# Kernel optimization log

Measured on AMD Instinct MI355X. Metric: run time of the kernel, lower is better.

Reference implementation:

```python
import jax, jax.numpy as jnp
import numpy as np

EPS = 1e-15
LRELU_ALPHA = 0.2  # = init alpha


def setup_inputs() -> dict:
    key = jax.random.key(0)
    k1, k2, k3, k4 = jax.random.split(key, 4)
    N, E, F_in, F_out = 100000, 3200000, 256, 64
    inputs = jax.random.normal(k1, (N, F_in), dtype=jnp.float32)
    edge_index = jax.random.randint(k2, (2, E), 0, N, dtype=jnp.int64)
    # xavier_normal with gain 1.414
    W = jax.random.normal(k3, (F_in, F_out), dtype=jnp.float32) * (1.414 * np.sqrt(2.0 / (F_in + F_out)))
    a = jax.random.normal(k4, (1, 2 * F_out), dtype=jnp.float32) * (1.414 * np.sqrt(2.0 / (1 + 2 * F_out)))
    return {"inputs": inputs, "edge_index": edge_index, "W": W, "a": a}


def reference(inputs, edge_index, W, a):
    N = inputs.shape[0]
    F_out = W.shape[1]
    src = edge_index[0]  # row i (destination of aggregation)
    dst = edge_index[1]  # col j (neighbor being aggregated)

    h = inputs @ W  # [N, F_out]
    # values = a @ concat(h[src], h[dst]).T  ==  (h @ a1)[src] + (h @ a2)[dst]
    a1 = a[0, :F_out]
    a2 = a[0, F_out:]
    s1 = h @ a1  # [N]
    s2 = h @ a2  # [N]
    values = s1[src] + s2[dst]  # [E]
    ev_a = jax.nn.leaky_relu(values, LRELU_ALPHA)
    edge_value = jnp.exp(ev_a - jnp.max(ev_a))  # global max, as in torch code

    # e_rowsum = A @ ones  -> per-row sum of edge values
    e_rowsum = jax.ops.segment_sum(edge_value, src, num_segments=N)  # [N]
    # h_prime = A @ h (dropout p=0 -> identity)
    h_prime = jax.ops.segment_sum(edge_value[:, None] * h[dst], src, num_segments=N)  # [N, F_out]
    h_prime = h_prime / (e_rowsum[:, None] + EPS)
    return jax.nn.elu(h_prime)  # concat=True
```

## Files before the change

### kernel.cpp

```cpp
#include <hip/hip_runtime.h>
#include <hip/hip_bf16.h>
#include <math.h>

#define F_IN 256
#define F_OUT 64
#define LRELU_ALPHA 0.2f
#define EPS 1e-15f
#define CHUNK 4096
#define BSH 7
#define BNODES 128
#define NBMAX 1024
#define LCAP 4800
#define CPAD 16

typedef __bf16 bf16x8 __attribute__((ext_vector_type(8)));
typedef float  f32x4  __attribute__((ext_vector_type(4)));

__device__ __forceinline__ unsigned int fkey(float x) {
    unsigned int u = __float_as_uint(x);
    return (u & 0x80000000u) ? ~u : (u | 0x80000000u);
}
__device__ __forceinline__ float funkey(unsigned int k) {
    return (k & 0x80000000u) ? __uint_as_float(k ^ 0x80000000u)
                             : __uint_as_float(~k);
}
__device__ __forceinline__ unsigned short f2bf(float x) {
    __hip_bfloat16 b = __float2bfloat16(x);
    return *reinterpret_cast<unsigned short*>(&b);
}
__device__ __forceinline__ float bf2f(unsigned int u) {
    return __uint_as_float(u << 16);
}

__global__ __launch_bounds__(256) void wprep(
    const float* __restrict__ W, unsigned short* __restrict__ Wt)
{
    const int i = blockIdx.x * 256 + threadIdx.x;
    const int n = i & 63;
    const int k = i >> 6;
    Wt[n * 256 + k] = f2bf(W[k * 64 + n]);
}

#define KAP 72
__global__ __launch_bounds__(256) void gemm_part(
    const float* __restrict__ X, const unsigned short* __restrict__ Wt,
    const float* __restrict__ a,
    unsigned short* __restrict__ h_bf, float* __restrict__ s1,
    float* __restrict__ s2, unsigned int* __restrict__ gsmax, int N,
    const int* __restrict__ src, const int* __restrict__ dst,
    int* __restrict__ coarse_cnt, unsigned int* __restrict__ coarse,
    int E, int NB, int GB)
{
    __shared__ __align__(16) char smem[18464];

    if (blockIdx.x < GB) {
        unsigned short* As = (unsigned short*)smem;
        float* red1 = (float*)(smem + 18432);
        float* red2 = red1 + 4;

        const int tid  = threadIdx.x;
        const int lane = tid & 63;
        const int l15  = lane & 15;
        const int quad = lane >> 4;
        const int w    = tid >> 6;
        const int n0   = blockIdx.x * 128;

        const unsigned short* wbase = Wt + l15 * 256 + quad * 8;

        f32x4 acc[2][4] = {};

        for (int c = 0; c < 4; ++c) {
            __syncthreads();
#pragma unroll
            for (int i = 0; i < 8; ++i) {
                int q   = tid + i * 256;
                int row = q >> 4;
                int k4  = q & 15;
                int gr  = n0 + row;
                float4 v = make_float4(0.f, 0.f, 0.f, 0.f);
                if (gr < N)
                    v = *(const float4*)&X[(size_t)gr * F_IN + c * 64 + k4 * 4];
                unsigned int p0 = f2bf(v.x) | ((unsigned int)f2bf(v.y) << 16);
                unsigned int p1 = f2bf(v.z) | ((unsigned int)f2bf(v.w) << 16);
                *(uint2*)&As[row * KAP + k4 * 4] = make_uint2(p0, p1);
            }
            __syncthreads();

#pragma unroll
            for (int ks = 0; ks < 64; ks += 32) {
                bf16x8 afrag[2], bfrag[4];
#pragma unroll
                for (int rt = 0; rt < 2; ++rt) {
                    uint4 ua = *(const uint4*)&As[(w * 32 + rt * 16 + l15) * KAP + ks + quad * 8];
                    afrag[rt] = __builtin_bit_cast(bf16x8, ua);
                }
#pragma unroll
                for (int ct = 0; ct < 4; ++ct) {
                    uint4 ub = *(const uint4*)&wbase[ct * 4096 + c * 64 + ks];
                    bfrag[ct] = __builtin_bit_cast(bf16x8, ub);
                }
#pragma unroll
                for (int rt = 0; rt < 2; ++rt)
#pragma unroll
                    for (int ct = 0; ct < 4; ++ct)
                        acc[rt][ct] = __builtin_amdgcn_mfma_f32_16x16x32_bf16(
                            afrag[rt], bfrag[ct], acc[rt][ct], 0, 0, 0);
            }
        }

        float a1v[4], a2v[4];
#pragma unroll
        for (int ct = 0; ct < 4; ++ct) {
            a1v[ct] = a[ct * 16 + l15];
            a2v[ct] = a[F_OUT + ct * 16 + l15];
        }
        float m1 = -INFINITY, m2 = -INFINITY;
#pragma unroll
        for (int rt = 0; rt < 2; ++rt) {
#pragma unroll
            for (int reg = 0; reg < 4; ++reg) {
                int n = n0 + w * 32 + rt * 16 + quad * 4 + reg;
                float p1 = 0.f, p2 = 0.f;
#pragma unroll
                for (int ct = 0; ct < 4; ++ct) {
                    float v = acc[rt][ct][reg];
                    p1 = fmaf(v, a1v[ct], p1);
                    p2 = fmaf(v, a2v[ct], p2);
                }
#pragma unroll
                for (int ofs = 1; ofs < 16; ofs <<= 1) {
                    p1 += __shfl_xor(p1, ofs, 64);
                    p2 += __shfl_xor(p2, ofs, 64);
                }
                if (n < N) {
#pragma unroll
                    for (int ct = 0; ct < 4; ++ct)
                        h_bf[(size_t)n * F_OUT + ct * 16 + l15] = f2bf(acc[rt][ct][reg]);
                    if (l15 == 0) { s1[n] = p1; s2[n] = p2; }
                    m1 = fmaxf(m1, p1);
                    m2 = fmaxf(m2, p2);
                }
            }
        }
#pragma unroll
        for (int ofs = 32; ofs > 0; ofs >>= 1) {
            m1 = fmaxf(m1, __shfl_xor(m1, ofs, 64));
            m2 = fmaxf(m2, __shfl_xor(m2, ofs, 64));
        }
        if (lane == 0) { red1[w] = m1; red2[w] = m2; }
        __syncthreads();
        if (tid == 0) {
            float b1 = fmaxf(fmaxf(red1[0], red1[1]), fmaxf(red1[2], red1[3]));
            float b2 = fmaxf(fmaxf(red2[0], red2[1]), fmaxf(red2[2], red2[3]));
            atomicMax(&gsmax[0], fkey(b1));
            atomicMax(&gsmax[1], fkey(b2));
        }
    } else {
        int* hist = (int*)smem;
        int* cur  = hist + NBMAX;
        const int pb = blockIdx.x - GB;
        const int e0 = pb * CHUNK;
        const int e1 = (e0 + CHUNK < E) ? e0 + CHUNK : E;
        const int nv = (e1 - e0) >> 2;
        const int4* s4p = (const int4*)(src + e0);
        const int4* d4p = (const int4*)(dst + e0);

        for (int i = threadIdx.x; i < NB; i += 256) hist[i] = 0;
        __syncthreads();

        for (int i = threadIdx.x; i < nv; i += 256) {
            int4 s4 = s4p[i];
            atomicAdd(&hist[s4.x >> BSH], 1);
            atomicAdd(&hist[s4.y >> BSH], 1);
            atomicAdd(&hist[s4.z >> BSH], 1);
            atomicAdd(&hist[s4.w >> BSH], 1);
        }
        for (int e = e0 + (nv << 2) + threadIdx.x; e < e1; e += 256)
            atomicAdd(&hist[src[e] >> BSH], 1);
        __syncthreads();

        for (int i = threadIdx.x; i < NB; i += 256) {
            int c = hist[i];
            cur[i] = c ? atomicAdd(&coarse_cnt[(size_t)i * CPAD], c) : 0;
        }
        __syncthreads();

        for (int i = threadIdx.x; i < nv; i += 256) {
            int4 s4 = s4p[i];
            int4 d4 = d4p[i];
#define PUT(S, D)                                                          \
            {                                                              \
                int b_   = (S) >> BSH;                                     \
                int pos_ = atomicAdd(&cur[b_], 1);                         \
                if (pos_ < LCAP)                                           \
                    coarse[(size_t)b_ * LCAP + pos_] =                     \
                        ((unsigned int)(D) << BSH) |                       \
                        (unsigned int)((S) & (BNODES - 1));                \
            }
            PUT(s4.x, d4.x)
            PUT(s4.y, d4.y)
            PUT(s4.z, d4.z)
            PUT(s4.w, d4.w)
        }
        for (int e = e0 + (nv << 2) + threadIdx.x; e < e1; e += 256) {
            int s = src[e], d = dst[e];
            PUT(s, d)
        }
#undef PUT
    }
}

__global__ __launch_bounds__(512) void bin_gather(
    const unsigned int* __restrict__ coarse, const int* __restrict__ coarse_cnt,
    const float* __restrict__ s1, const float* __restrict__ s2,
    const unsigned int* __restrict__ gsmax,
    const unsigned short* __restrict__ hb, float* __restrict__ out, int N)
{
    __shared__ unsigned int leds[LCAP];
    __shared__ int   hcnt[BNODES];
    __shared__ int   hinc[BNODES];
    __shared__ int   curs[BNODES];
    __shared__ float s1s[BNODES];

    const int b  = blockIdx.x;
    const int t  = threadIdx.x;
    const int n0 = b << BSH;
    int cnt = coarse_cnt[(size_t)b * CPAD];
    if (cnt > LCAP) cnt = LCAP;
    const unsigned int* cb = coarse + (size_t)b * LCAP;

    if (t < BNODES) {
        hcnt[t] = 0;
        s1s[t] = (n0 + t < N) ? s1[n0 + t] : 0.f;
    }
    __syncthreads();

    for (int e = t; e < cnt; e += 512)
        atomicAdd(&hcnt[cb[e] & (BNODES - 1)], 1);
    __syncthreads();

    if (t < BNODES) hinc[t] = hcnt[t];
    __syncthreads();
    for (int d = 1; d < BNODES; d <<= 1) {
        int x = (t < BNODES && t >= d) ? hinc[t - d] : 0;
        __syncthreads();
        if (t < BNODES) hinc[t] += x;
        __syncthreads();
    }
    if (t < BNODES) curs[t] = hinc[t] - hcnt[t];
    __syncthreads();

    const float M = funkey(gsmax[0]) + funkey(gsmax[1]);
    for (int e = t; e < cnt; e += 512) {
        unsigned int p = cb[e];
        int sl = p & (BNODES - 1);
        int d  = p >> BSH;
        float v = s1s[sl] + s2[d];
        v = fmaxf(v, LRELU_ALPHA * v);
        float w = __expf(v - M);
        unsigned int wb = f2bf(w);
        int pos = atomicAdd(&curs[sl], 1);
        leds[pos] = ((unsigned int)d << 15) | wb;
    }
    __syncthreads();

    const int lane = t & 63;
    const int wv   = t >> 6;
    const int g    = lane >> 4;
    const int fi   = lane & 15;

    for (int i = 0; i < 16; ++i) {
        const int nl = wv * 16 + i;
        const int n  = n0 + nl;
        const bool valid = (n < N);
        const int re = valid ? hinc[nl] : 0;
        const int rs = valid ? re - hcnt[nl] : 0;

        float a0 = 0.f, a1 = 0.f, a2 = 0.f, a3 = 0.f, ws = 0.f;
        for (int bb = rs; bb < re; bb += 64) {
            const int nb = (re - bb < 64) ? re - bb : 64;
            unsigned int pv = (lane < nb) ? leds[bb + lane] : 0u;
            ws += bf2f(pv & 0x7fffu);
            for (int k = 0; k < nb; k += 4) {
                unsigned int pe = __shfl(pv, k + g, 64);
                float w = bf2f(pe & 0x7fffu);
                uint2 hv = *(const uint2*)&hb[(size_t)(pe >> 15) * F_OUT + fi * 4];
                a0 = fmaf(w, bf2f(hv.x & 0xffffu), a0);
                a1 = fmaf(w, bf2f(hv.x >> 16),     a1);
                a2 = fmaf(w, bf2f(hv.y & 0xffffu), a2);
                a3 = fmaf(w, bf2f(hv.y >> 16),     a3);
            }
        }
        a0 += __shfl_xor(a0, 16, 64); a0 += __shfl_xor(a0, 32, 64);
        a1 += __shfl_xor(a1, 16, 64); a1 += __shfl_xor(a1, 32, 64);
        a2 += __shfl_xor(a2, 16, 64); a2 += __shfl_xor(a2, 32, 64);
        a3 += __shfl_xor(a3, 16, 64); a3 += __shfl_xor(a3, 32, 64);
#pragma unroll
        for (int ofs = 32; ofs > 0; ofs >>= 1)
            ws += __shfl_xor(ws, ofs, 64);

        if (valid && g == 0) {
            float inv = 1.f / (ws + EPS);
            float x0 = a0 * inv, x1 = a1 * inv, x2 = a2 * inv, x3 = a3 * inv;
            x0 = (x0 > 0.f) ? x0 : expm1f(x0);
            x1 = (x1 > 0.f) ? x1 : expm1f(x1);
            x2 = (x2 > 0.f) ? x2 : expm1f(x2);
            x3 = (x3 > 0.f) ? x3 : expm1f(x3);
            *(float4*)&out[(size_t)n * F_OUT + fi * 4] = make_float4(x0, x1, x2, x3);
        }
    }
}

extern "C" void kernel_launch(void* const* d_in, const int* in_sizes, int n_in,
                              void* d_out, int out_size, void* d_ws, size_t ws_size,
                              hipStream_t stream) {
    const float* X   = (const float*)d_in[0];
    const int*   ei  = (const int*)d_in[1];
    const float* W   = (const float*)d_in[2];
    const float* a   = (const float*)d_in[3];
    float*       out = (float*)d_out;

    const int N = in_sizes[0] / F_IN;
    const int E = in_sizes[1] / 2;
    const int* src = ei;
    const int* dst = ei + E;

    const int NB = (N + BNODES - 1) >> BSH;
    const int GB = (N + 127) / 128;
    const int PB = (E + CHUNK - 1) / CHUNK;

    unsigned short* h_bf = (unsigned short*)d_ws;
    float* s1         = (float*)(h_bf + (size_t)N * F_OUT);
    float* s2         = s1 + N;
    int*   coarse_cnt = (int*)(s2 + N);
    unsigned int* gsmax = (unsigned int*)(coarse_cnt + (size_t)NB * CPAD);
    unsigned short* Wt = (unsigned short*)(gsmax + 2);
    unsigned int* coarse = (unsigned int*)(Wt + 64 * 256);

    hipMemsetAsync(coarse_cnt, 0, ((size_t)NB * CPAD + 2) * sizeof(int), stream);

    wprep     <<<64, 256, 0, stream>>>(W, Wt);
    gemm_part <<<GB + PB, 256, 0, stream>>>(X, Wt, a, h_bf, s1, s2, gsmax, N,
                                            src, dst, coarse_cnt, coarse,
                                            E, NB, GB);
    bin_gather<<<NB, 512, 0, stream>>>(coarse, coarse_cnt, s1, s2, gsmax,
                                       h_bf, out, N);
}
```

Before: 332.2 us.

## Unroll gather loads, batch edge weights, reorder blocks, rotate bin atomics

The neighbor-gather loop now handles four edges per step, so four independent h row loads are in flight per lane before any FMAs use them. The edge-weight pass processes two edges per thread per iteration and issues both s2 loads up front. In the fused first kernel, edge-partition blocks now come before GEMM blocks, and each partition block starts its coarse_cnt atomic reservations at a different rotation to spread contention across bins. Costs are more registers and redundant loads of hb[0] for padding lanes, which are harmless because their weight is zero.

```diff
diff --git a/kernel.cpp b/kernel.cpp
--- a/kernel.cpp
+++ b/kernel.cpp
@@ -49,11 +49,11 @@
     float* __restrict__ s2, unsigned int* __restrict__ gsmax, int N,
     const int* __restrict__ src, const int* __restrict__ dst,
     int* __restrict__ coarse_cnt, unsigned int* __restrict__ coarse,
-    int E, int NB, int GB)
+    int E, int NB, int PB)
 {
     __shared__ __align__(16) char smem[18464];
 
-    if (blockIdx.x < GB) {
+    if (blockIdx.x >= PB) {
         unsigned short* As = (unsigned short*)smem;
         float* red1 = (float*)(smem + 18432);
         float* red2 = red1 + 4;
@@ -63,7 +63,7 @@
         const int l15  = lane & 15;
         const int quad = lane >> 4;
         const int w    = tid >> 6;
-        const int n0   = blockIdx.x * 128;
+        const int n0   = (blockIdx.x - PB) * 128;
 
         const unsigned short* wbase = Wt + l15 * 256 + quad * 8;
 
@@ -158,7 +158,7 @@
     } else {
         int* hist = (int*)smem;
         int* cur  = hist + NBMAX;
-        const int pb = blockIdx.x - GB;
+        const int pb = blockIdx.x;
         const int e0 = pb * CHUNK;
         const int e1 = (e0 + CHUNK < E) ? e0 + CHUNK : E;
         const int nv = (e1 - e0) >> 2;
@@ -179,9 +179,14 @@
             atomicAdd(&hist[src[e] >> BSH], 1);
         __syncthreads();
 
-        for (int i = threadIdx.x; i < NB; i += 256) {
-            int c = hist[i];
-            cur[i] = c ? atomicAdd(&coarse_cnt[(size_t)i * CPAD], c) : 0;
+        {
+            const int rot = (pb * 389) % NB;
+            for (int i = threadIdx.x; i < NB; i += 256) {
+                int j = i + rot;
+                if (j >= NB) j -= NB;
+                int c = hist[j];
+                cur[j] = c ? atomicAdd(&coarse_cnt[(size_t)j * CPAD], c) : 0;
+            }
         }
         __syncthreads();
 
@@ -251,16 +256,30 @@
     __syncthreads();
 
     const float M = funkey(gsmax[0]) + funkey(gsmax[1]);
-    for (int e = t; e < cnt; e += 512) {
-        unsigned int p = cb[e];
-        int sl = p & (BNODES - 1);
-        int d  = p >> BSH;
-        float v = s1s[sl] + s2[d];
-        v = fmaxf(v, LRELU_ALPHA * v);
-        float w = __expf(v - M);
-        unsigned int wb = f2bf(w);
-        int pos = atomicAdd(&curs[sl], 1);
-        leds[pos] = ((unsigned int)d << 15) | wb;
+    for (int e = t; e < cnt; e += 1024) {
+        unsigned int p0 = cb[e];
+        const int e2 = e + 512;
+        const bool h2 = (e2 < cnt);
+        unsigned int p1 = h2 ? cb[e2] : 0u;
+        float sa = s2[p0 >> BSH];
+        float sb = h2 ? s2[p1 >> BSH] : 0.f;
+
+        {
+            int sl = p0 & (BNODES - 1);
+            float v = s1s[sl] + sa;
+            v = fmaxf(v, LRELU_ALPHA * v);
+            unsigned int wb = f2bf(__expf(v - M));
+            int pos = atomicAdd(&curs[sl], 1);
+            leds[pos] = ((p0 >> BSH) << 15) | wb;
+        }
+        if (h2) {
+            int sl = p1 & (BNODES - 1);
+            float v = s1s[sl] + sb;
+            v = fmaxf(v, LRELU_ALPHA * v);
+            unsigned int wb = f2bf(__expf(v - M));
+            int pos = atomicAdd(&curs[sl], 1);
+            leds[pos] = ((p1 >> BSH) << 15) | wb;
+        }
     }
     __syncthreads();
 
@@ -281,14 +300,35 @@
             const int nb = (re - bb < 64) ? re - bb : 64;
             unsigned int pv = (lane < nb) ? leds[bb + lane] : 0u;
             ws += bf2f(pv & 0x7fffu);
-            for (int k = 0; k < nb; k += 4) {
-                unsigned int pe = __shfl(pv, k + g, 64);
-                float w = bf2f(pe & 0x7fffu);
-                uint2 hv = *(const uint2*)&hb[(size_t)(pe >> 15) * F_OUT + fi * 4];
-                a0 = fmaf(w, bf2f(hv.x & 0xffffu), a0);
-                a1 = fmaf(w, bf2f(hv.x >> 16),     a1);
-                a2 = fmaf(w, bf2f(hv.y & 0xffffu), a2);
-                a3 = fmaf(w, bf2f(hv.y >> 16),     a3);
+            for (int k = 0; k < nb; k += 16) {
+                unsigned int pe0 = __shfl(pv, k + g,      64);
+                unsigned int pe1 = __shfl(pv, k + 4 + g,  64);
+                unsigned int pe2 = __shfl(pv, k + 8 + g,  64);
+                unsigned int pe3 = __shfl(pv, k + 12 + g, 64);
+                float w0 = bf2f(pe0 & 0x7fffu);
+                float w1 = bf2f(pe1 & 0x7fffu);
+                float w2 = bf2f(pe2 & 0x7fffu);
+                float w3 = bf2f(pe3 & 0x7fffu);
+                uint2 hv0 = *(const uint2*)&hb[(size_t)(pe0 >> 15) * F_OUT + fi * 4];
+                uint2 hv1 = *(const uint2*)&hb[(size_t)(pe1 >> 15) * F_OUT + fi * 4];
+                uint2 hv2 = *(const uint2*)&hb[(size_t)(pe2 >> 15) * F_OUT + fi * 4];
+                uint2 hv3 = *(const uint2*)&hb[(size_t)(pe3 >> 15) * F_OUT + fi * 4];
+                a0 = fmaf(w0, bf2f(hv0.x & 0xffffu), a0);
+                a1 = fmaf(w0, bf2f(hv0.x >> 16),     a1);
+                a2 = fmaf(w0, bf2f(hv0.y & 0xffffu), a2);
+                a3 = fmaf(w0, bf2f(hv0.y >> 16),     a3);
+                a0 = fmaf(w1, bf2f(hv1.x & 0xffffu), a0);
+                a1 = fmaf(w1, bf2f(hv1.x >> 16),     a1);
+                a2 = fmaf(w1, bf2f(hv1.y & 0xffffu), a2);
+                a3 = fmaf(w1, bf2f(hv1.y >> 16),     a3);
+                a0 = fmaf(w2, bf2f(hv2.x & 0xffffu), a0);
+                a1 = fmaf(w2, bf2f(hv2.x >> 16),     a1);
+                a2 = fmaf(w2, bf2f(hv2.y & 0xffffu), a2);
+                a3 = fmaf(w2, bf2f(hv2.y >> 16),     a3);
+                a0 = fmaf(w3, bf2f(hv3.x & 0xffffu), a0);
+                a1 = fmaf(w3, bf2f(hv3.x >> 16),     a1);
+                a2 = fmaf(w3, bf2f(hv3.y & 0xffffu), a2);
+                a3 = fmaf(w3, bf2f(hv3.y >> 16),     a3);
             }
         }
         a0 += __shfl_xor(a0, 16, 64); a0 += __shfl_xor(a0, 32, 64);
@@ -340,9 +380,9 @@
     hipMemsetAsync(coarse_cnt, 0, ((size_t)NB * CPAD + 2) * sizeof(int), stream);
 
     wprep     <<<64, 256, 0, stream>>>(W, Wt);
-    gemm_part <<<GB + PB, 256, 0, stream>>>(X, Wt, a, h_bf, s1, s2, gsmax, N,
+    gemm_part <<<PB + GB, 256, 0, stream>>>(X, Wt, a, h_bf, s1, s2, gsmax, N,
                                             src, dst, coarse_cnt, coarse,
-                                            E, NB, GB);
+                                            E, NB, PB);
     bin_gather<<<NB, 512, 0, stream>>>(coarse, coarse_cnt, s1, s2, gsmax,
                                        h_bf, out, N);
 }
```

After: 346.9 us. 4.4% more time.
